# Kernel optimization log

Hardware: AMD Instinct MI355X
Metric: run time of the kernel (lower is better)

## Reference

```python
import jax, jax.numpy as jnp
import numpy as np

DIM_PER_HEAD = 64
NEG_BIG = -1e9


def setup_inputs() -> dict:
    key = jax.random.key(0)
    kq, kk, kv, km = jax.random.split(key, 4)
    B, H, S, D = 2, 16, 2048, DIM_PER_HEAD
    Q = jax.random.normal(kq, (B, H, S, D), dtype=jnp.float32)
    K = jax.random.normal(kk, (B, H, S, D), dtype=jnp.float32)
    V = jax.random.normal(kv, (B, H, S, D), dtype=jnp.float32)
    attn_mask = jax.random.randint(km, (B, 1, S, S), 0, 2).astype(jnp.bool_)
    return {"Q": Q, "K": K, "V": V, "attn_mask": attn_mask}


def reference(Q, K, V, attn_mask):
    scale = 1.0 / np.sqrt(DIM_PER_HEAD).astype(np.float32)
    # [B,H,S,S] scores = Q @ K^T / sqrt(d)
    scores = jnp.einsum("bhqd,bhkd->bhqk", Q, K) * scale
    scores = jnp.where(attn_mask, NEG_BIG, scores)
    attn = jax.nn.softmax(scores, axis=-1)
    context = jnp.einsum("bhqk,bhkd->bhqd", attn, V)
    return (context, attn)
```

## Files before the change

kernel.cpp:

```cpp
#include <hip/hip_runtime.h>

#define S_LEN  2048
#define DH     64
#define NHEAD  16
#define NBATCH 2
#define SCALE  0.125f
#define NEG_BIG (-1e9f)

typedef short bf16x8 __attribute__((ext_vector_type(8)));
typedef float f32x4  __attribute__((ext_vector_type(4)));

static __device__ __forceinline__ short f2b(float f) {
  return __builtin_bit_cast(short, (__bf16)f);
}
static __device__ __forceinline__ bf16x8 pack8(float4 a, float4 b) {
  bf16x8 r;
  r[0] = f2b(a.x); r[1] = f2b(a.y); r[2] = f2b(a.z); r[3] = f2b(a.w);
  r[4] = f2b(b.x); r[5] = f2b(b.y); r[6] = f2b(b.z); r[7] = f2b(b.w);
  return r;
}
static __device__ __forceinline__ unsigned int packbf2(float lo, float hi) {
  unsigned short l = __builtin_bit_cast(unsigned short, (__bf16)lo);
  unsigned short h = __builtin_bit_cast(unsigned short, (__bf16)hi);
  return ((unsigned int)h << 16) | (unsigned int)l;
}

__global__ __launch_bounds__(256, 3)
void sdpa_mfma(const float* __restrict__ Qg, const float* __restrict__ Kg,
               const float* __restrict__ Vg, const int* __restrict__ Mg,
               float* __restrict__ ctx_g, float* __restrict__ attn_g) {
  __shared__ __align__(16) short Kb[64 * 64];
  __shared__ __align__(16) short Vt[64 * 64];
  __shared__ __align__(16) float Ps[64 * 68];

  const int tid  = threadIdx.x;
  const int w    = tid >> 6;
  const int lane = tid & 63;
  const int l15  = lane & 15;
  const int quad = lane >> 4;
  const int q0 = blockIdx.x * 64;
  const int h  = blockIdx.y;
  const int b  = blockIdx.z;

  const size_t head = (size_t)(b * NHEAD + h);
  const float* Qh = Qg + head * S_LEN * DH;
  const float* Kh = Kg + head * S_LEN * DH;
  const float* Vh = Vg + head * S_LEN * DH;
  const int*   Mb = Mg + (size_t)b * S_LEN * S_LEN;
  float* ctxh  = ctx_g  + head * S_LEN * DH;
  float* attnh = attn_g + head * S_LEN * S_LEN;

  bf16x8 aq0, aq1;
  {
    const float* qp = Qh + (size_t)(q0 + 16 * w + l15) * DH + (quad << 3);
    float4 f0 = *(const float4*)(qp);
    float4 f1 = *(const float4*)(qp + 4);
    float4 f2 = *(const float4*)(qp + 32);
    float4 f3 = *(const float4*)(qp + 36);
    aq0 = pack8(f0, f1);
    aq1 = pack8(f2, f3);
  }

  const int* mrow[4];
  float* arow[4];
  #pragma unroll
  for (int reg = 0; reg < 4; ++reg) {
    int grow = q0 + 16 * w + 4 * quad + reg;
    mrow[reg] = Mb + (size_t)grow * S_LEN + l15;
    arow[reg] = attnh + (size_t)grow * S_LEN + l15;
  }

  const int srow = tid >> 2, sseg = tid & 3;
  const int vp = tid >> 3, vcb = (tid & 7) << 3;

  float lsum[4] = {0.f, 0.f, 0.f, 0.f};

  for (int k0 = 0; k0 < S_LEN; k0 += 64) {
    __syncthreads();
    {
      const float* kp = Kh + (size_t)(k0 + srow) * DH + (sseg << 4);
      float4 a = ((const float4*)kp)[0];
      float4 c = ((const float4*)kp)[1];
      float4 d = ((const float4*)kp)[2];
      float4 e = ((const float4*)kp)[3];
      int base = srow << 6, x = srow & 7;
      *(bf16x8*)&Kb[base + ((((sseg << 1)    ) ^ x) << 3)] = pack8(a, c);
      *(bf16x8*)&Kb[base + ((((sseg << 1) | 1) ^ x) << 3)] = pack8(d, e);
    }
    __syncthreads();

    f32x4 sc[4];
    #pragma unroll
    for (int jt = 0; jt < 4; ++jt) {
      int row = (jt << 4) + l15, x = l15 & 7;
      bf16x8 b0 = *(const bf16x8*)&Kb[(row << 6) + (((quad    ) ^ x) << 3)];
      bf16x8 b1 = *(const bf16x8*)&Kb[(row << 6) + (((quad | 4) ^ x) << 3)];
      f32x4 acc = {0.f, 0.f, 0.f, 0.f};
      acc = __builtin_amdgcn_mfma_f32_16x16x32_bf16(aq0, b0, acc, 0, 0, 0);
      acc = __builtin_amdgcn_mfma_f32_16x16x32_bf16(aq1, b1, acc, 0, 0, 0);
      sc[jt] = acc;
    }

    int mv[4][4];
    #pragma unroll
    for (int reg = 0; reg < 4; ++reg)
      #pragma unroll
      for (int jt = 0; jt < 4; ++jt)
        mv[reg][jt] = mrow[reg][k0 + (jt << 4)];

    #pragma unroll
    for (int reg = 0; reg < 4; ++reg)
      #pragma unroll
      for (int jt = 0; jt < 4; ++jt) {
        float s = mv[reg][jt] ? NEG_BIG : sc[jt][reg] * SCALE;
        lsum[reg] += __expf(s);
      }
  }

  float invl[4];
  #pragma unroll
  for (int reg = 0; reg < 4; ++reg) {
    float t = lsum[reg];
    t += __shfl_xor(t, 1);
    t += __shfl_xor(t, 2);
    t += __shfl_xor(t, 4);
    t += __shfl_xor(t, 8);
    invl[reg] = 1.0f / t;
  }

  f32x4 cacc[4];
  #pragma unroll
  for (int jt = 0; jt < 4; ++jt) cacc[jt] = (f32x4){0.f, 0.f, 0.f, 0.f};

  for (int k0 = 0; k0 < S_LEN; k0 += 64) {
    __syncthreads();
    {
      const float* kp = Kh + (size_t)(k0 + srow) * DH + (sseg << 4);
      float4 a = ((const float4*)kp)[0];
      float4 c = ((const float4*)kp)[1];
      float4 d = ((const float4*)kp)[2];
      float4 e = ((const float4*)kp)[3];
      int base = srow << 6, x = srow & 7;
      *(bf16x8*)&Kb[base + ((((sseg << 1)    ) ^ x) << 3)] = pack8(a, c);
      *(bf16x8*)&Kb[base + ((((sseg << 1) | 1) ^ x) << 3)] = pack8(d, e);

      const float* v0 = Vh + (size_t)(k0 + 2 * vp) * DH + vcb;
      const float* v1 = v0 + DH;
      float4 a0 = ((const float4*)v0)[0], a1 = ((const float4*)v0)[1];
      float4 b0 = ((const float4*)v1)[0], b1 = ((const float4*)v1)[1];
      float lo[8] = {a0.x, a0.y, a0.z, a0.w, a1.x, a1.y, a1.z, a1.w};
      float hi[8] = {b0.x, b0.y, b0.z, b0.w, b1.x, b1.y, b1.z, b1.w};
      int ch = vp >> 2, wi = (vp & 3) << 1;
      #pragma unroll
      for (int c = 0; c < 8; ++c) {
        int dd = vcb + c;
        *(unsigned int*)&Vt[(dd << 6) + ((ch ^ (dd & 7)) << 3) + wi] =
            packbf2(lo[c], hi[c]);
      }
    }
    __syncthreads();

    f32x4 sc[4];
    #pragma unroll
    for (int jt = 0; jt < 4; ++jt) {
      int row = (jt << 4) + l15, x = l15 & 7;
      bf16x8 b0 = *(const bf16x8*)&Kb[(row << 6) + (((quad    ) ^ x) << 3)];
      bf16x8 b1 = *(const bf16x8*)&Kb[(row << 6) + (((quad | 4) ^ x) << 3)];
      f32x4 acc = {0.f, 0.f, 0.f, 0.f};
      acc = __builtin_amdgcn_mfma_f32_16x16x32_bf16(aq0, b0, acc, 0, 0, 0);
      acc = __builtin_amdgcn_mfma_f32_16x16x32_bf16(aq1, b1, acc, 0, 0, 0);
      sc[jt] = acc;
    }

    int mv[4][4];
    #pragma unroll
    for (int reg = 0; reg < 4; ++reg)
      #pragma unroll
      for (int jt = 0; jt < 4; ++jt)
        mv[reg][jt] = mrow[reg][k0 + (jt << 4)];

    #pragma unroll
    for (int reg = 0; reg < 4; ++reg) {
      float* prow = &Ps[(16 * w + 4 * quad + reg) * 68 + l15];
      #pragma unroll
      for (int jt = 0; jt < 4; ++jt) {
        float s = mv[reg][jt] ? NEG_BIG : sc[jt][reg] * SCALE;
        float p = __expf(s) * invl[reg];
        arow[reg][k0 + (jt << 4)] = p;
        prow[jt << 4] = p;
      }
    }
    bf16x8 ap0, ap1;
    {
      const float* pp = &Ps[(16 * w + l15) * 68 + (quad << 3)];
      float4 p0 = *(const float4*)(pp);
      float4 p1 = *(const float4*)(pp + 4);
      float4 p2 = *(const float4*)(pp + 32);
      float4 p3 = *(const float4*)(pp + 36);
      ap0 = pack8(p0, p1);
      ap1 = pack8(p2, p3);
    }
    #pragma unroll
    for (int jt = 0; jt < 4; ++jt) {
      int d = (jt << 4) + l15, x = l15 & 7;
      bf16x8 bv0 = *(const bf16x8*)&Vt[(d << 6) + (((quad    ) ^ x) << 3)];
      bf16x8 bv1 = *(const bf16x8*)&Vt[(d << 6) + (((quad | 4) ^ x) << 3)];
      cacc[jt] = __builtin_amdgcn_mfma_f32_16x16x32_bf16(ap0, bv0, cacc[jt], 0, 0, 0);
      cacc[jt] = __builtin_amdgcn_mfma_f32_16x16x32_bf16(ap1, bv1, cacc[jt], 0, 0, 0);
    }
  }

  #pragma unroll
  for (int reg = 0; reg < 4; ++reg) {
    float* crow = ctxh + (size_t)(q0 + 16 * w + 4 * quad + reg) * DH + l15;
    #pragma unroll
    for (int jt = 0; jt < 4; ++jt)
      crow[jt << 4] = cacc[jt][reg];
  }
}

extern "C" void kernel_launch(void* const* d_in, const int* in_sizes, int n_in,
                              void* d_out, int out_size, void* d_ws, size_t ws_size,
                              hipStream_t stream) {
  (void)in_sizes; (void)n_in; (void)d_ws; (void)ws_size; (void)out_size;
  const float* Q = (const float*)d_in[0];
  const float* K = (const float*)d_in[1];
  const float* V = (const float*)d_in[2];
  const int*   M = (const int*)d_in[3];
  float* ctx  = (float*)d_out;
  float* attn = ctx + (size_t)NBATCH * NHEAD * S_LEN * DH;
  dim3 grid(S_LEN / 64, NHEAD, NBATCH);
  sdpa_mfma<<<grid, dim3(256), 0, stream>>>(Q, K, V, M, ctx, attn);
}
```

Before: 791.5 us.

## Split first-pass row-sum across warps by key range and prefetch K/V tiles

The first pass that computes softmax denominators is restructured. Each warp now covers all 64 query rows over its own quarter of the keys, loading K straight from global memory instead of through shared memory with barriers, and the partial sums are combined through a small shared buffer. The second pass prefetches the next K/V tile into registers while computing the current one, raises wave priority around the MFMA blocks, and writes the attention and context outputs with nontemporal stores. Occupancy is raised from 3 to 4 blocks per SM, which adds register pressure because each thread now holds all Q fragments and 16 partial sums.

```diff
diff --git a/kernel.cpp b/kernel.cpp
--- a/kernel.cpp
+++ b/kernel.cpp
@@ -25,13 +25,14 @@
   return ((unsigned int)h << 16) | (unsigned int)l;
 }
 
-__global__ __launch_bounds__(256, 3)
+__global__ __launch_bounds__(256, 4)
 void sdpa_mfma(const float* __restrict__ Qg, const float* __restrict__ Kg,
                const float* __restrict__ Vg, const int* __restrict__ Mg,
                float* __restrict__ ctx_g, float* __restrict__ attn_g) {
   __shared__ __align__(16) short Kb[64 * 64];
   __shared__ __align__(16) short Vt[64 * 64];
   __shared__ __align__(16) float Ps[64 * 68];
+  __shared__ float Lred[4 * 64];
 
   const int tid  = threadIdx.x;
   const int w    = tid >> 6;
@@ -50,46 +51,126 @@
   float* ctxh  = ctx_g  + head * S_LEN * DH;
   float* attnh = attn_g + head * S_LEN * S_LEN;
 
-  bf16x8 aq0, aq1;
+  bf16x8 aqA[4], aqB[4];
+  #pragma unroll
+  for (int rg = 0; rg < 4; ++rg) {
+    const float* qp = Qh + (size_t)(q0 + 16 * rg + l15) * DH + (quad << 3);
+    float4 f0 = ((const float4*)qp)[0];
+    float4 f1 = ((const float4*)qp)[1];
+    float4 f2 = ((const float4*)qp)[8];
+    float4 f3 = ((const float4*)qp)[9];
+    aqA[rg] = pack8(f0, f1);
+    aqB[rg] = pack8(f2, f3);
+  }
+
+  float lsum[16] = {0.f};
   {
-    const float* qp = Qh + (size_t)(q0 + 16 * w + l15) * DH + (quad << 3);
-    float4 f0 = *(const float4*)(qp);
-    float4 f1 = *(const float4*)(qp + 4);
-    float4 f2 = *(const float4*)(qp + 32);
-    float4 f3 = *(const float4*)(qp + 36);
-    aq0 = pack8(f0, f1);
-    aq1 = pack8(f2, f3);
-  }
-
-  const int* mrow[4];
-  float* arow[4];
-  #pragma unroll
-  for (int reg = 0; reg < 4; ++reg) {
-    int grow = q0 + 16 * w + 4 * quad + reg;
-    mrow[reg] = Mb + (size_t)grow * S_LEN + l15;
-    arow[reg] = attnh + (size_t)grow * S_LEN + l15;
-  }
+    const int* mb1 = Mb + (size_t)(q0 + 4 * quad) * S_LEN + l15;
+    const int kw = w << 9;
+    for (int it = 0; it < 8; ++it) {
+      const int k0 = kw + (it << 6);
+      #pragma unroll
+      for (int jt = 0; jt < 4; ++jt) {
+        const float* kp = Kh + (size_t)(k0 + (jt << 4) + l15) * DH + (quad << 3);
+        float4 f0 = ((const float4*)kp)[0];
+        float4 f1 = ((const float4*)kp)[1];
+        float4 f2 = ((const float4*)kp)[8];
+        float4 f3 = ((const float4*)kp)[9];
+        bf16x8 b0 = pack8(f0, f1);
+        bf16x8 b1 = pack8(f2, f3);
+
+        int mv[16];
+        #pragma unroll
+        for (int i = 0; i < 16; ++i)
+          mv[i] = mb1[(16 * (i >> 2) + (i & 3)) * S_LEN + k0 + (jt << 4)];
+
+        #pragma unroll
+        for (int rg = 0; rg < 4; ++rg) {
+          f32x4 acc = {0.f, 0.f, 0.f, 0.f};
+          acc = __builtin_amdgcn_mfma_f32_16x16x32_bf16(aqA[rg], b0, acc, 0, 0, 0);
+          acc = __builtin_amdgcn_mfma_f32_16x16x32_bf16(aqB[rg], b1, acc, 0, 0, 0);
+          #pragma unroll
+          for (int reg = 0; reg < 4; ++reg) {
+            float s = mv[rg * 4 + reg] ? NEG_BIG : acc[reg] * SCALE;
+            lsum[rg * 4 + reg] += __expf(s);
+          }
+        }
+      }
+    }
+  }
+
+  #pragma unroll
+  for (int i = 0; i < 16; ++i) {
+    float t = lsum[i];
+    t += __shfl_xor(t, 1);
+    t += __shfl_xor(t, 2);
+    t += __shfl_xor(t, 4);
+    t += __shfl_xor(t, 8);
+    if (l15 == 0) Lred[(w << 6) + 16 * (i >> 2) + 4 * quad + (i & 3)] = t;
+  }
+  __syncthreads();
 
   const int srow = tid >> 2, sseg = tid & 3;
   const int vp = tid >> 3, vcb = (tid & 7) << 3;
-
-  float lsum[4] = {0.f, 0.f, 0.f, 0.f};
+  float4 pkA, pkB, pkC, pkD, pva, pvb, pvc, pvd;
+  #define LOADK(K0) do { \
+    const float* kp_ = Kh + (size_t)((K0) + srow) * DH + (sseg << 4); \
+    pkA = ((const float4*)kp_)[0]; pkB = ((const float4*)kp_)[1]; \
+    pkC = ((const float4*)kp_)[2]; pkD = ((const float4*)kp_)[3]; } while (0)
+  #define LOADV(K0) do { \
+    const float* v0_ = Vh + (size_t)((K0) + 2 * vp) * DH + vcb; \
+    pva = ((const float4*)v0_)[0]; pvb = ((const float4*)v0_)[1]; \
+    pvc = ((const float4*)(v0_ + DH))[0]; pvd = ((const float4*)(v0_ + DH))[1]; } while (0)
+  LOADK(0);
+  LOADV(0);
+
+  float invl[4];
+  #pragma unroll
+  for (int reg = 0; reg < 4; ++reg) {
+    int r = 16 * w + 4 * quad + reg;
+    invl[reg] = 1.0f / (Lred[r] + Lred[64 + r] + Lred[128 + r] + Lred[192 + r]);
+  }
+
+  bf16x8 aq0, aq1;
+  if      (w == 0) { aq0 = aqA[0]; aq1 = aqB[0]; }
+  else if (w == 1) { aq0 = aqA[1]; aq1 = aqB[1]; }
+  else if (w == 2) { aq0 = aqA[2]; aq1 = aqB[2]; }
+  else             { aq0 = aqA[3]; aq1 = aqB[3]; }
+
+  f32x4 cacc[4];
+  #pragma unroll
+  for (int jt = 0; jt < 4; ++jt) cacc[jt] = (f32x4){0.f, 0.f, 0.f, 0.f};
+
+  const int* mb2 = Mb + (size_t)(q0 + 16 * w + 4 * quad) * S_LEN + l15;
+  float* ab = attnh + (size_t)(q0 + 16 * w + 4 * quad) * S_LEN + l15;
 
   for (int k0 = 0; k0 < S_LEN; k0 += 64) {
     __syncthreads();
     {
-      const float* kp = Kh + (size_t)(k0 + srow) * DH + (sseg << 4);
-      float4 a = ((const float4*)kp)[0];
-      float4 c = ((const float4*)kp)[1];
-      float4 d = ((const float4*)kp)[2];
-      float4 e = ((const float4*)kp)[3];
       int base = srow << 6, x = srow & 7;
-      *(bf16x8*)&Kb[base + ((((sseg << 1)    ) ^ x) << 3)] = pack8(a, c);
-      *(bf16x8*)&Kb[base + ((((sseg << 1) | 1) ^ x) << 3)] = pack8(d, e);
+      *(bf16x8*)&Kb[base + ((((sseg << 1)    ) ^ x) << 3)] = pack8(pkA, pkB);
+      *(bf16x8*)&Kb[base + ((((sseg << 1) | 1) ^ x) << 3)] = pack8(pkC, pkD);
+
+      float lo[8] = {pva.x, pva.y, pva.z, pva.w, pvb.x, pvb.y, pvb.z, pvb.w};
+      float hi[8] = {pvc.x, pvc.y, pvc.z, pvc.w, pvd.x, pvd.y, pvd.z, pvd.w};
+      int ch = vp >> 2, wi = (vp & 3) << 1;
+      #pragma unroll
+      for (int c = 0; c < 8; ++c) {
+        int dd = vcb + c;
+        *(unsigned int*)&Vt[(dd << 6) + ((ch ^ (dd & 7)) << 3) + wi] =
+            packbf2(lo[c], hi[c]);
+      }
     }
     __syncthreads();
+    if (k0 + 64 < S_LEN) { LOADK(k0 + 64); LOADV(k0 + 64); }
+
+    int mv[16];
+    #pragma unroll
+    for (int i = 0; i < 16; ++i)
+      mv[i] = mb2[(i >> 2) * S_LEN + k0 + ((i & 3) << 4)];
 
     f32x4 sc[4];
+    __builtin_amdgcn_s_setprio(1);
     #pragma unroll
     for (int jt = 0; jt < 4; ++jt) {
       int row = (jt << 4) + l15, x = l15 & 7;
@@ -100,106 +181,31 @@
       acc = __builtin_amdgcn_mfma_f32_16x16x32_bf16(aq1, b1, acc, 0, 0, 0);
       sc[jt] = acc;
     }
-
-    int mv[4][4];
-    #pragma unroll
-    for (int reg = 0; reg < 4; ++reg)
-      #pragma unroll
-      for (int jt = 0; jt < 4; ++jt)
-        mv[reg][jt] = mrow[reg][k0 + (jt << 4)];
-
-    #pragma unroll
-    for (int reg = 0; reg < 4; ++reg)
-      #pragma unroll
-      for (int jt = 0; jt < 4; ++jt) {
-        float s = mv[reg][jt] ? NEG_BIG : sc[jt][reg] * SCALE;
-        lsum[reg] += __expf(s);
-      }
-  }
-
-  float invl[4];
-  #pragma unroll
-  for (int reg = 0; reg < 4; ++reg) {
-    float t = lsum[reg];
-    t += __shfl_xor(t, 1);
-    t += __shfl_xor(t, 2);
-    t += __shfl_xor(t, 4);
-    t += __shfl_xor(t, 8);
-    invl[reg] = 1.0f / t;
-  }
-
-  f32x4 cacc[4];
-  #pragma unroll
-  for (int jt = 0; jt < 4; ++jt) cacc[jt] = (f32x4){0.f, 0.f, 0.f, 0.f};
-
-  for (int k0 = 0; k0 < S_LEN; k0 += 64) {
-    __syncthreads();
-    {
-      const float* kp = Kh + (size_t)(k0 + srow) * DH + (sseg << 4);
-      float4 a = ((const float4*)kp)[0];
-      float4 c = ((const float4*)kp)[1];
-      float4 d = ((const float4*)kp)[2];
-      float4 e = ((const float4*)kp)[3];
-      int base = srow << 6, x = srow & 7;
-      *(bf16x8*)&Kb[base + ((((sseg << 1)    ) ^ x) << 3)] = pack8(a, c);
-      *(bf16x8*)&Kb[base + ((((sseg << 1) | 1) ^ x) << 3)] = pack8(d, e);
-
-      const float* v0 = Vh + (size_t)(k0 + 2 * vp) * DH + vcb;
-      const float* v1 = v0 + DH;
-      float4 a0 = ((const float4*)v0)[0], a1 = ((const float4*)v0)[1];
-      float4 b0 = ((const float4*)v1)[0], b1 = ((const float4*)v1)[1];
-      float lo[8] = {a0.x, a0.y, a0.z, a0.w, a1.x, a1.y, a1.z, a1.w};
-      float hi[8] = {b0.x, b0.y, b0.z, b0.w, b1.x, b1.y, b1.z, b1.w};
-      int ch = vp >> 2, wi = (vp & 3) << 1;
-      #pragma unroll
-      for (int c = 0; c < 8; ++c) {
-        int dd = vcb + c;
-        *(unsigned int*)&Vt[(dd << 6) + ((ch ^ (dd & 7)) << 3) + wi] =
-            packbf2(lo[c], hi[c]);
-      }
-    }
-    __syncthreads();
-
-    f32x4 sc[4];
-    #pragma unroll
-    for (int jt = 0; jt < 4; ++jt) {
-      int row = (jt << 4) + l15, x = l15 & 7;
-      bf16x8 b0 = *(const bf16x8*)&Kb[(row << 6) + (((quad    ) ^ x) << 3)];
-      bf16x8 b1 = *(const bf16x8*)&Kb[(row << 6) + (((quad | 4) ^ x) << 3)];
-      f32x4 acc = {0.f, 0.f, 0.f, 0.f};
-      acc = __builtin_amdgcn_mfma_f32_16x16x32_bf16(aq0, b0, acc, 0, 0, 0);
-      acc = __builtin_amdgcn_mfma_f32_16x16x32_bf16(aq1, b1, acc, 0, 0, 0);
-      sc[jt] = acc;
-    }
-
-    int mv[4][4];
-    #pragma unroll
-    for (int reg = 0; reg < 4; ++reg)
-      #pragma unroll
-      for (int jt = 0; jt < 4; ++jt)
-        mv[reg][jt] = mrow[reg][k0 + (jt << 4)];
+    __builtin_amdgcn_s_setprio(0);
 
     #pragma unroll
     for (int reg = 0; reg < 4; ++reg) {
       float* prow = &Ps[(16 * w + 4 * quad + reg) * 68 + l15];
       #pragma unroll
       for (int jt = 0; jt < 4; ++jt) {
-        float s = mv[reg][jt] ? NEG_BIG : sc[jt][reg] * SCALE;
+        float s = mv[reg * 4 + jt] ? NEG_BIG : sc[jt][reg] * SCALE;
         float p = __expf(s) * invl[reg];
-        arow[reg][k0 + (jt << 4)] = p;
+        __builtin_nontemporal_store(p, &ab[(reg * S_LEN) + k0 + (jt << 4)]);
         prow[jt << 4] = p;
       }
     }
+
     bf16x8 ap0, ap1;
     {
       const float* pp = &Ps[(16 * w + l15) * 68 + (quad << 3)];
-      float4 p0 = *(const float4*)(pp);
-      float4 p1 = *(const float4*)(pp + 4);
-      float4 p2 = *(const float4*)(pp + 32);
-      float4 p3 = *(const float4*)(pp + 36);
+      float4 p0 = ((const float4*)pp)[0];
+      float4 p1 = ((const float4*)pp)[1];
+      float4 p2 = ((const float4*)pp)[8];
+      float4 p3 = ((const float4*)pp)[9];
       ap0 = pack8(p0, p1);
       ap1 = pack8(p2, p3);
     }
+    __builtin_amdgcn_s_setprio(1);
     #pragma unroll
     for (int jt = 0; jt < 4; ++jt) {
       int d = (jt << 4) + l15, x = l15 & 7;
@@ -208,6 +214,7 @@
       cacc[jt] = __builtin_amdgcn_mfma_f32_16x16x32_bf16(ap0, bv0, cacc[jt], 0, 0, 0);
       cacc[jt] = __builtin_amdgcn_mfma_f32_16x16x32_bf16(ap1, bv1, cacc[jt], 0, 0, 0);
     }
+    __builtin_amdgcn_s_setprio(0);
   }
 
   #pragma unroll
@@ -215,7 +222,7 @@
     float* crow = ctxh + (size_t)(q0 + 16 * w + 4 * quad + reg) * DH + l15;
     #pragma unroll
     for (int jt = 0; jt < 4; ++jt)
-      crow[jt << 4] = cacc[jt][reg];
+      __builtin_nontemporal_store(cacc[jt][reg], &crow[jt << 4]);
   }
 }
 
```

After: 886.4 us. +12.0%, slower.

## Prefetch next K/V/mask tiles into registers and use nontemporal attn stores

Applied to the files above, without the earlier changes.

Software-pipelines global loads of K, V and the mask for the next 64-key tile into registers while the current tile is computed, so global latency overlaps with MFMA and exp work. It also replaces __expf with exp2 on scores pre-multiplied by log2(e), raises wave priority around the MFMA blocks, and writes the large attention matrix and the context with nontemporal stores to limit cache pollution. The register prefetch raises VGPR pressure, which could cut occupancy under the 3-blocks-per-SM launch bound.

```diff
diff --git a/kernel.cpp b/kernel.cpp
--- a/kernel.cpp
+++ b/kernel.cpp
@@ -5,6 +5,7 @@
 #define NHEAD  16
 #define NBATCH 2
 #define SCALE  0.125f
+#define L2E_SC 0.18033688011112042f
 #define NEG_BIG (-1e9f)
 
 typedef short bf16x8 __attribute__((ext_vector_type(8)));
@@ -49,47 +50,62 @@
   const int*   Mb = Mg + (size_t)b * S_LEN * S_LEN;
   float* ctxh  = ctx_g  + head * S_LEN * DH;
   float* attnh = attn_g + head * S_LEN * S_LEN;
+  const ptrdiff_t dAM = (const char*)attnh - (const char*)Mb;
 
   bf16x8 aq0, aq1;
   {
     const float* qp = Qh + (size_t)(q0 + 16 * w + l15) * DH + (quad << 3);
-    float4 f0 = *(const float4*)(qp);
-    float4 f1 = *(const float4*)(qp + 4);
-    float4 f2 = *(const float4*)(qp + 32);
-    float4 f3 = *(const float4*)(qp + 36);
-    aq0 = pack8(f0, f1);
-    aq1 = pack8(f2, f3);
+    aq0 = pack8(((const float4*)qp)[0], ((const float4*)qp)[1]);
+    aq1 = pack8(((const float4*)qp)[8], ((const float4*)qp)[9]);
   }
 
   const int* mrow[4];
-  float* arow[4];
   #pragma unroll
   for (int reg = 0; reg < 4; ++reg) {
     int grow = q0 + 16 * w + 4 * quad + reg;
     mrow[reg] = Mb + (size_t)grow * S_LEN + l15;
-    arow[reg] = attnh + (size_t)grow * S_LEN + l15;
   }
 
   const int srow = tid >> 2, sseg = tid & 3;
   const int vp = tid >> 3, vcb = (tid & 7) << 3;
 
+  float4 pkA, pkB, pkC, pkD, pva, pvb, pvc, pvd;
+  int mvc[16];
+
+#define LOADK(K0) do { \
+    const float* kp_ = Kh + (size_t)((K0) + srow) * DH + (sseg << 4); \
+    pkA = ((const float4*)kp_)[0]; pkB = ((const float4*)kp_)[1]; \
+    pkC = ((const float4*)kp_)[2]; pkD = ((const float4*)kp_)[3]; } while (0)
+#define LOADV(K0) do { \
+    const float* v0_ = Vh + (size_t)((K0) + 2 * vp) * DH + vcb; \
+    pva = ((const float4*)v0_)[0]; pvb = ((const float4*)v0_)[1]; \
+    pvc = ((const float4*)(v0_ + DH))[0]; pvd = ((const float4*)(v0_ + DH))[1]; } while (0)
+#define LOADM(K0) do { \
+    mvc[0]  = mrow[0][(K0)];      mvc[1]  = mrow[0][(K0) + 16]; \
+    mvc[2]  = mrow[0][(K0) + 32]; mvc[3]  = mrow[0][(K0) + 48]; \
+    mvc[4]  = mrow[1][(K0)];      mvc[5]  = mrow[1][(K0) + 16]; \
+    mvc[6]  = mrow[1][(K0) + 32]; mvc[7]  = mrow[1][(K0) + 48]; \
+    mvc[8]  = mrow[2][(K0)];      mvc[9]  = mrow[2][(K0) + 16]; \
+    mvc[10] = mrow[2][(K0) + 32]; mvc[11] = mrow[2][(K0) + 48]; \
+    mvc[12] = mrow[3][(K0)];      mvc[13] = mrow[3][(K0) + 16]; \
+    mvc[14] = mrow[3][(K0) + 32]; mvc[15] = mrow[3][(K0) + 48]; } while (0)
+#define STOREK() do { \
+    int base_ = srow << 6, x_ = srow & 7; \
+    *(bf16x8*)&Kb[base_ + ((((sseg << 1)    ) ^ x_) << 3)] = pack8(pkA, pkB); \
+    *(bf16x8*)&Kb[base_ + ((((sseg << 1) | 1) ^ x_) << 3)] = pack8(pkC, pkD); } while (0)
+
   float lsum[4] = {0.f, 0.f, 0.f, 0.f};
+  LOADK(0);
+  LOADM(0);
 
   for (int k0 = 0; k0 < S_LEN; k0 += 64) {
     __syncthreads();
-    {
-      const float* kp = Kh + (size_t)(k0 + srow) * DH + (sseg << 4);
-      float4 a = ((const float4*)kp)[0];
-      float4 c = ((const float4*)kp)[1];
-      float4 d = ((const float4*)kp)[2];
-      float4 e = ((const float4*)kp)[3];
-      int base = srow << 6, x = srow & 7;
-      *(bf16x8*)&Kb[base + ((((sseg << 1)    ) ^ x) << 3)] = pack8(a, c);
-      *(bf16x8*)&Kb[base + ((((sseg << 1) | 1) ^ x) << 3)] = pack8(d, e);
-    }
-    __syncthreads();
+    STOREK();
+    __syncthreads();
+    if (k0 + 64 < S_LEN) LOADK(k0 + 64);
 
     f32x4 sc[4];
+    __builtin_amdgcn_s_setprio(1);
     #pragma unroll
     for (int jt = 0; jt < 4; ++jt) {
       int row = (jt << 4) + l15, x = l15 & 7;
@@ -100,21 +116,16 @@
       acc = __builtin_amdgcn_mfma_f32_16x16x32_bf16(aq1, b1, acc, 0, 0, 0);
       sc[jt] = acc;
     }
-
-    int mv[4][4];
-    #pragma unroll
-    for (int reg = 0; reg < 4; ++reg)
-      #pragma unroll
-      for (int jt = 0; jt < 4; ++jt)
-        mv[reg][jt] = mrow[reg][k0 + (jt << 4)];
+    __builtin_amdgcn_s_setprio(0);
 
     #pragma unroll
     for (int reg = 0; reg < 4; ++reg)
       #pragma unroll
       for (int jt = 0; jt < 4; ++jt) {
-        float s = mv[reg][jt] ? NEG_BIG : sc[jt][reg] * SCALE;
-        lsum[reg] += __expf(s);
+        float t = mvc[reg * 4 + jt] ? NEG_BIG : sc[jt][reg] * L2E_SC;
+        lsum[reg] += __builtin_amdgcn_exp2f(t);
       }
+    if (k0 + 64 < S_LEN) LOADM(k0 + 64);
   }
 
   float invl[4];
@@ -132,24 +143,16 @@
   #pragma unroll
   for (int jt = 0; jt < 4; ++jt) cacc[jt] = (f32x4){0.f, 0.f, 0.f, 0.f};
 
+  LOADK(0);
+  LOADV(0);
+  LOADM(0);
+
   for (int k0 = 0; k0 < S_LEN; k0 += 64) {
     __syncthreads();
+    STOREK();
     {
-      const float* kp = Kh + (size_t)(k0 + srow) * DH + (sseg << 4);
-      float4 a = ((const float4*)kp)[0];
-      float4 c = ((const float4*)kp)[1];
-      float4 d = ((const float4*)kp)[2];
-      float4 e = ((const float4*)kp)[3];
-      int base = srow << 6, x = srow & 7;
-      *(bf16x8*)&Kb[base + ((((sseg << 1)    ) ^ x) << 3)] = pack8(a, c);
-      *(bf16x8*)&Kb[base + ((((sseg << 1) | 1) ^ x) << 3)] = pack8(d, e);
-
-      const float* v0 = Vh + (size_t)(k0 + 2 * vp) * DH + vcb;
-      const float* v1 = v0 + DH;
-      float4 a0 = ((const float4*)v0)[0], a1 = ((const float4*)v0)[1];
-      float4 b0 = ((const float4*)v1)[0], b1 = ((const float4*)v1)[1];
-      float lo[8] = {a0.x, a0.y, a0.z, a0.w, a1.x, a1.y, a1.z, a1.w};
-      float hi[8] = {b0.x, b0.y, b0.z, b0.w, b1.x, b1.y, b1.z, b1.w};
+      float lo[8] = {pva.x, pva.y, pva.z, pva.w, pvb.x, pvb.y, pvb.z, pvb.w};
+      float hi[8] = {pvc.x, pvc.y, pvc.z, pvc.w, pvd.x, pvd.y, pvd.z, pvd.w};
       int ch = vp >> 2, wi = (vp & 3) << 1;
       #pragma unroll
       for (int c = 0; c < 8; ++c) {
@@ -159,8 +162,10 @@
       }
     }
     __syncthreads();
+    if (k0 + 64 < S_LEN) { LOADK(k0 + 64); LOADV(k0 + 64); }
 
     f32x4 sc[4];
+    __builtin_amdgcn_s_setprio(1);
     #pragma unroll
     for (int jt = 0; jt < 4; ++jt) {
       int row = (jt << 4) + l15, x = l15 & 7;
@@ -171,35 +176,29 @@
       acc = __builtin_amdgcn_mfma_f32_16x16x32_bf16(aq1, b1, acc, 0, 0, 0);
       sc[jt] = acc;
     }
-
-    int mv[4][4];
-    #pragma unroll
-    for (int reg = 0; reg < 4; ++reg)
-      #pragma unroll
-      for (int jt = 0; jt < 4; ++jt)
-        mv[reg][jt] = mrow[reg][k0 + (jt << 4)];
+    __builtin_amdgcn_s_setprio(0);
 
     #pragma unroll
     for (int reg = 0; reg < 4; ++reg) {
       float* prow = &Ps[(16 * w + 4 * quad + reg) * 68 + l15];
+      float* arow = (float*)((char*)mrow[reg] + dAM);
       #pragma unroll
       for (int jt = 0; jt < 4; ++jt) {
-        float s = mv[reg][jt] ? NEG_BIG : sc[jt][reg] * SCALE;
-        float p = __expf(s) * invl[reg];
-        arow[reg][k0 + (jt << 4)] = p;
+        float t = mvc[reg * 4 + jt] ? NEG_BIG : sc[jt][reg] * L2E_SC;
+        float p = __builtin_amdgcn_exp2f(t) * invl[reg];
+        __builtin_nontemporal_store(p, &arow[k0 + (jt << 4)]);
         prow[jt << 4] = p;
       }
     }
+    if (k0 + 64 < S_LEN) LOADM(k0 + 64);
+
     bf16x8 ap0, ap1;
     {
       const float* pp = &Ps[(16 * w + l15) * 68 + (quad << 3)];
-      float4 p0 = *(const float4*)(pp);
-      float4 p1 = *(const float4*)(pp + 4);
-      float4 p2 = *(const float4*)(pp + 32);
-      float4 p3 = *(const float4*)(pp + 36);
-      ap0 = pack8(p0, p1);
-      ap1 = pack8(p2, p3);
-    }
+      ap0 = pack8(((const float4*)pp)[0], ((const float4*)pp)[1]);
+      ap1 = pack8(((const float4*)pp)[8], ((const float4*)pp)[9]);
+    }
+    __builtin_amdgcn_s_setprio(1);
     #pragma unroll
     for (int jt = 0; jt < 4; ++jt) {
       int d = (jt << 4) + l15, x = l15 & 7;
@@ -208,6 +207,7 @@
       cacc[jt] = __builtin_amdgcn_mfma_f32_16x16x32_bf16(ap0, bv0, cacc[jt], 0, 0, 0);
       cacc[jt] = __builtin_amdgcn_mfma_f32_16x16x32_bf16(ap1, bv1, cacc[jt], 0, 0, 0);
     }
+    __builtin_amdgcn_s_setprio(0);
   }
 
   #pragma unroll
@@ -215,7 +215,7 @@
     float* crow = ctxh + (size_t)(q0 + 16 * w + 4 * quad + reg) * DH + l15;
     #pragma unroll
     for (int jt = 0; jt < 4; ++jt)
-      crow[jt << 4] = cacc[jt][reg];
+      __builtin_nontemporal_store(cacc[jt][reg], &crow[jt << 4]);
   }
 }
 
```

After: 774.2 us. 2.2% less time.
